# Performance work log

Hardware: AMD Instinct MI355X
Metric: run time of the kernel (lower is better)

## Reference

```python
import jax, jax.numpy as jnp
import numpy as np

N_HEAD, D_K, D_MODEL = 8, 64, 512  # factorized_k == d_k == d_v forced by view()/einsum consistency
B, LQ, LK = 4, 2048, 2048
TEMP = float(np.sqrt(D_K))
NEG = -1000000000.0


def setup_inputs() -> dict:
    key = jax.random.key(0)
    ks = jax.random.split(key, 8)
    q = jax.random.normal(ks[0], (B, LQ, D_MODEL), jnp.float32)
    k = jax.random.normal(ks[1], (B, LK, D_MODEL), jnp.float32)
    v = jax.random.normal(ks[2], (B, LK, D_MODEL), jnp.float32)
    mask = jax.random.randint(ks[3], (B, LQ, LK), 0, 2).astype(jnp.int32)
    # torch.rand-style positive uniform params, scaled to keep the 4-matmul chain O(1)
    W_A = jax.random.uniform(ks[4], (D_MODEL, D_K), jnp.float32, 0.0, 1.0 / D_K)
    W_A2 = jax.random.uniform(ks[5], (D_MODEL, D_K), jnp.float32, 0.0, 1.0 / D_K)
    W_A3 = jax.random.uniform(ks[6], (D_MODEL, D_K), jnp.float32, 0.0, 1.0 / D_K)
    fc_w = jax.random.normal(ks[7], (D_MODEL, N_HEAD * D_K), jnp.float32) / np.float32(np.sqrt(N_HEAD * D_K))
    ln_gamma = jnp.ones((D_MODEL,), jnp.float32)
    ln_beta = jnp.zeros((D_MODEL,), jnp.float32)
    return dict(q=q, k=k, v=v, mask=mask, W_A=W_A, W_A2=W_A2, W_A3=W_A3,
                fc_w=fc_w, ln_gamma=ln_gamma, ln_beta=ln_beta)


def reference(q, k, v, mask, W_A, W_A2, W_A3, fc_w, ln_gamma, ln_beta):
    b, lq, dm = q.shape
    lk = k.shape[1]
    residual = q
    # Since factorized_k == d_k, view(n_head,d_k,-1) and view(n_head,-1,d_k) coincide.
    W_a = W_A.reshape(N_HEAD, D_K, D_K)    # plays both 'bcd' (W_A) and 'bdi' (W_B)
    W_a2 = W_A2.reshape(N_HEAD, D_K, D_K)  # plays both 'bim' (W_At) and 'bmj' (W_Bt)
    W_av = W_A3.reshape(N_HEAD, D_K, D_K)  # plays both 'bna' (W_av) and 'bac' (W_bv)

    kt = jnp.swapaxes(k, 1, 2).reshape(b, N_HEAD, D_K, lk)  # [b,h,dk,lk]
    qh = q.reshape(b, lq, N_HEAD, D_K)                       # [b,lq,h,dk]
    vh = v.reshape(b, lk, N_HEAD, D_K)                       # [b,lk,h,dk]

    # Fold the tiny per-head weight chain first (same math as the 6-tensor einsum).
    Wq = jnp.einsum('hcd,hdi,him,hmj->hcj', W_a, W_a, W_a2, W_a2)  # [h,dk,dk]
    attn = jnp.einsum('kahc,hcj,khjn->khan', qh, Wq, kt) / TEMP     # [b,h,lq,lk]
    attn = jnp.where(mask[:, None, :, :] != 0, attn, NEG)
    attn = jax.nn.softmax(attn, axis=-1)  # dropout is identity in eval

    Wv = jnp.einsum('hna,hac->hnc', W_av, W_av)                    # [h,dk,dk]
    out = jnp.einsum('khjm,kmhn,hnc->khjc', attn, vh, Wv)          # [b,h,lq,dk]
    out = jnp.swapaxes(out, 1, 2).reshape(b, lq, N_HEAD * D_K)
    out = out @ fc_w.T  # Linear bias=False; dropout identity
    out = out + residual
    mu = jnp.mean(out, axis=-1, keepdims=True)
    var = jnp.mean((out - mu) ** 2, axis=-1, keepdims=True)
    out = (out - mu) / jnp.sqrt(var + 1e-6) * ln_gamma + ln_beta
    return (out, attn)
```

## Files before the change

### kernel.cpp

```cpp
#include <hip/hip_runtime.h>

#define B_ 4
#define H_ 8
#define L_ 2048
#define DM 512
#define DK 64

typedef __bf16 bf16x8 __attribute__((ext_vector_type(8)));
typedef float f32x4 __attribute__((ext_vector_type(4)));

__device__ __forceinline__ f32x4 mfma16(bf16x8 a, bf16x8 b, f32x4 c) {
  return __builtin_amdgcn_mfma_f32_16x16x32_bf16(a, b, c, 0, 0, 0);
}
__device__ __forceinline__ unsigned short f2bf(float f) {
  unsigned int u = __float_as_uint(f);
  u += 0x7fffu + ((u >> 16) & 1u);
  return (unsigned short)(u >> 16);
}
__device__ __forceinline__ void async16(const void* g, void* l) {
  __builtin_amdgcn_global_load_lds((const __attribute__((address_space(1))) unsigned int*)g,
                                   (__attribute__((address_space(3))) unsigned int*)l, 16, 0, 0);
}
__device__ __forceinline__ float rsum16(float v) {
  v += __shfl_xor(v, 1);
  v += __shfl_xor(v, 2);
  v += __shfl_xor(v, 4);
  v += __shfl_xor(v, 8);
  return v;
}

__device__ __forceinline__ void mm64(const float* X, const float* Y, float acc[4][4], int tr, int tc) {
#pragma unroll
  for (int rr = 0; rr < 4; ++rr)
#pragma unroll
    for (int cc = 0; cc < 4; ++cc) acc[rr][cc] = 0.f;
  for (int c = 0; c < 64; ++c) {
    float a0 = X[(tr + 0) * 65 + c], a1 = X[(tr + 1) * 65 + c];
    float a2 = X[(tr + 2) * 65 + c], a3 = X[(tr + 3) * 65 + c];
    float b0 = Y[c * 65 + tc + 0], b1 = Y[c * 65 + tc + 1];
    float b2 = Y[c * 65 + tc + 2], b3 = Y[c * 65 + tc + 3];
    acc[0][0] += a0 * b0; acc[0][1] += a0 * b1; acc[0][2] += a0 * b2; acc[0][3] += a0 * b3;
    acc[1][0] += a1 * b0; acc[1][1] += a1 * b1; acc[1][2] += a1 * b2; acc[1][3] += a1 * b3;
    acc[2][0] += a2 * b0; acc[2][1] += a2 * b1; acc[2][2] += a2 * b2; acc[2][3] += a2 * b3;
    acc[3][0] += a3 * b0; acc[3][1] += a3 * b1; acc[3][2] += a3 * b2; acc[3][3] += a3 * b3;
  }
}

__global__ __launch_bounds__(256) void k_weights(const float* __restrict__ WA, const float* __restrict__ WA2,
                                                 const float* __restrict__ WA3, float* __restrict__ Wq,
                                                 float* __restrict__ Wv) {
  __shared__ float sA[64 * 65], sB[64 * 65], sT[64 * 65];
  const int h = blockIdx.x, t = threadIdx.x;
  const int tr = (t >> 4) * 4, tc = (t & 15) * 4;
  for (int i = t; i < 4096; i += 256) {
    int r = i >> 6, c = i & 63;
    sA[r * 65 + c] = WA[h * 4096 + i];
    sB[r * 65 + c] = WA2[h * 4096 + i];
  }
  __syncthreads();
  float acc[4][4];
  mm64(sA, sA, acc, tr, tc);
#pragma unroll
  for (int rr = 0; rr < 4; ++rr)
#pragma unroll
    for (int cc = 0; cc < 4; ++cc) sT[(tr + rr) * 65 + tc + cc] = acc[rr][cc];
  __syncthreads();
  mm64(sT, sB, acc, tr, tc);
#pragma unroll
  for (int rr = 0; rr < 4; ++rr)
#pragma unroll
    for (int cc = 0; cc < 4; ++cc) sA[(tr + rr) * 65 + tc + cc] = acc[rr][cc];
  __syncthreads();
  mm64(sA, sB, acc, tr, tc);
#pragma unroll
  for (int rr = 0; rr < 4; ++rr)
#pragma unroll
    for (int cc = 0; cc < 4; ++cc) Wq[h * 4096 + (tr + rr) * 64 + tc + cc] = acc[rr][cc];
  for (int i = t; i < 4096; i += 256) {
    int r = i >> 6, c = i & 63;
    sT[r * 65 + c] = WA3[h * 4096 + i];
  }
  __syncthreads();
  mm64(sT, sT, acc, tr, tc);
#pragma unroll
  for (int rr = 0; rr < 4; ++rr)
#pragma unroll
    for (int cc = 0; cc < 4; ++cc) Wv[h * 4096 + (tr + rr) * 64 + tc + cc] = acc[rr][cc];
}

__global__ void k_conv(const float* __restrict__ s, unsigned short* __restrict__ d, int n4) {
  int i = blockIdx.x * blockDim.x + threadIdx.x;
  int stride = gridDim.x * blockDim.x;
  for (; i < n4; i += stride) {
    float4 f = ((const float4*)s)[i];
    ushort4 o;
    o.x = f2bf(f.x); o.y = f2bf(f.y); o.z = f2bf(f.z); o.w = f2bf(f.w);
    ((ushort4*)d)[i] = o;
  }
}

__global__ __launch_bounds__(256) void k_maskpack(const int* __restrict__ mask,
                                                  unsigned long long* __restrict__ mp) {
  const int row = blockIdx.x * 4 + (threadIdx.x >> 6);
  const int lane = threadIdx.x & 63;
  const int* src = mask + (size_t)row * L_;
#pragma unroll
  for (int c = 0; c < 32; ++c) {
    int mv = src[c * 64 + lane];
    unsigned long long bits = __ballot(mv != 0);
    if (lane == 0) mp[(size_t)row * 32 + c] = bits;
  }
}

__global__ __launch_bounds__(256) void k_qprime(const float* __restrict__ q, const float* __restrict__ Wq,
                                                unsigned short* __restrict__ Qp) {
  __shared__ float sW[64 * 65], sQ[64 * 65];
  const int bid = blockIdx.x;
  const int rt = bid & 31, h = (bid >> 5) & 7, b = bid >> 8;
  const int t = threadIdx.x;
  const int row0 = rt * 64;
  for (int i = t; i < 4096; i += 256) {
    int r = i >> 6, c = i & 63;
    sW[r * 65 + c] = Wq[h * 4096 + i];
    sQ[r * 65 + c] = q[(size_t)(b * L_ + row0 + r) * DM + h * DK + c];
  }
  __syncthreads();
  float acc[4][4];
  const int tr = (t >> 4) * 4, tc = (t & 15) * 4;
  mm64(sQ, sW, acc, tr, tc);
#pragma unroll
  for (int rr = 0; rr < 4; ++rr) {
    ushort4 o;
    o.x = f2bf(acc[rr][0] * 0.125f); o.y = f2bf(acc[rr][1] * 0.125f);
    o.z = f2bf(acc[rr][2] * 0.125f); o.w = f2bf(acc[rr][3] * 0.125f);
    *(ushort4*)&Qp[(size_t)(b * L_ + row0 + tr + rr) * DM + h * DK + tc] = o;
  }
}

__global__ __launch_bounds__(256) void k_vprime(const float* __restrict__ v, const float* __restrict__ Wv,
                                                unsigned short* __restrict__ VpT) {
  __shared__ float sW[64 * 65], sV[64 * 65];
  __shared__ __align__(16) unsigned short ldsT[64 * 72];
  const int bid = blockIdx.x;
  const int rt = bid & 31, h = (bid >> 5) & 7, b = bid >> 8;
  const int t = threadIdx.x;
  const int key0 = rt * 64;
  for (int i = t; i < 4096; i += 256) {
    int r = i >> 6, c = i & 63;
    sW[r * 65 + c] = Wv[h * 4096 + i];
    sV[r * 65 + c] = v[(size_t)(b * L_ + key0 + r) * DM + h * DK + c];
  }
  __syncthreads();
  float acc[4][4];
  const int tr = (t >> 4) * 4, tc = (t & 15) * 4;
  mm64(sV, sW, acc, tr, tc);
#pragma unroll
  for (int rr = 0; rr < 4; ++rr)
#pragma unroll
    for (int cc = 0; cc < 4; ++cc) ldsT[(tc + cc) * 72 + tr + rr] = f2bf(acc[rr][cc]);
  __syncthreads();
  const int dk = t >> 2, kc = t & 3;
  const uint4* srcp = (const uint4*)&ldsT[dk * 72 + kc * 16];
  uint4 v0 = srcp[0], v1 = srcp[1];
  size_t go = ((size_t)((b * H_ + h) * DK + dk)) * L_ + key0 + kc * 16;
  *(uint4*)&VpT[go] = v0;
  *(uint4*)&VpT[go + 8] = v1;
}

__global__ __launch_bounds__(256) void k_attn(const unsigned short* __restrict__ Qp,
                                              const unsigned short* __restrict__ Kb,
                                              const unsigned short* __restrict__ VpT,
                                              const unsigned long long* __restrict__ mp,
                                              float* __restrict__ attn,
                                              float* __restrict__ ov) {
  __shared__ __align__(16) unsigned short KT[2][4096];
  __shared__ __align__(16) unsigned short VT[2][4096];
  __shared__ __align__(16) unsigned short PB[4][16 * 76];
  const int bid0 = blockIdx.x;
  const int bid = (bid0 & 7) * 128 + (bid0 >> 3);
  const int qt = bid & 31;
  const int h = (bid >> 5) & 7;
  const int b = bid >> 8;
  const int tid = threadIdx.x;
  const int lane = tid & 63;
  const int w = tid >> 6;
  const int l15 = lane & 15, l4 = lane >> 4;
  const int row0 = qt * 64 + w * 16;

  const unsigned short* qb = Qp + ((size_t)(b * L_ + row0 + l15)) * DM + h * DK + l4 * 8;
  const bf16x8 aQ0 = *(const bf16x8*)qb;
  const bf16x8 aQ1 = *(const bf16x8*)(qb + 32);

  const size_t kb_base = (size_t)b * L_ * DM + h * DK;
  const size_t vt_base = (size_t)((b * H_ + h) * DK) * L_;
  const unsigned long long* mrow = mp + (size_t)(b * L_ + row0 + l4 * 4) * 32;

  const int p_lo = tid * 16;
  const int skey = p_lo >> 7;
  const int sboff = (p_lo & 127) ^ ((skey & 7) << 4);
  const int skey1 = (p_lo + 4096) >> 7;
  const int sboff1 = ((p_lo + 4096) & 127) ^ ((skey1 & 7) << 4);

#define STAGE_K(kt_, s_)                                                                   \
  {                                                                                        \
    async16(Kb + kb_base + (size_t)((kt_) * 64 + skey) * DM + (sboff >> 1),                \
            (char*)&KT[s_][0] + p_lo);                                                     \
    async16(Kb + kb_base + (size_t)((kt_) * 64 + skey1) * DM + (sboff1 >> 1),              \
            (char*)&KT[s_][0] + p_lo + 4096);                                              \
  }
#define STAGE_V(kt_, s_)                                                                   \
  {                                                                                        \
    async16(VpT + vt_base + (size_t)skey * L_ + (kt_) * 64 + (sboff >> 1),                 \
            (char*)&VT[s_][0] + p_lo);                                                     \
    async16(VpT + vt_base + (size_t)skey1 * L_ + (kt_) * 64 + (sboff1 >> 1),               \
            (char*)&VT[s_][0] + p_lo + 4096);                                              \
  }

  float lsum[4] = {0.f, 0.f, 0.f, 0.f};

  STAGE_K(0, 0);
  __syncthreads();
  for (int kt = 0; kt < 32; ++kt) {
    const int cur = kt & 1;
    if (kt < 31) STAGE_K(kt + 1, cur ^ 1);
    unsigned long long mw[4];
#pragma unroll
    for (int r = 0; r < 4; ++r) mw[r] = mrow[r * 32 + kt];
    const char* Kbase = (const char*)&KT[cur][0];
#pragma unroll
    for (int f = 0; f < 4; ++f) {
      int keyrow = f * 16 + l15;
      int sw = (keyrow & 7) << 4;
      bf16x8 b0 = *(const bf16x8*)(Kbase + keyrow * 128 + ((l4 * 16) ^ sw));
      bf16x8 b1 = *(const bf16x8*)(Kbase + keyrow * 128 + ((64 + l4 * 16) ^ sw));
      f32x4 acc = {0.f, 0.f, 0.f, 0.f};
      acc = mfma16(aQ0, b0, acc);
      acc = mfma16(aQ1, b1, acc);
#pragma unroll
      for (int r = 0; r < 4; ++r) {
        unsigned int hb = (unsigned int)(mw[r] >> (f * 16));
        lsum[r] += ((hb >> l15) & 1u) ? __expf(acc[r]) : 0.f;
      }
    }
    __syncthreads();
  }
  float invl[4];
#pragma unroll
  for (int r = 0; r < 4; ++r) invl[r] = 1.0f / rsum16(lsum[r]);

  f32x4 O[4];
#pragma unroll
  for (int d = 0; d < 4; ++d) { f32x4 z = {0.f, 0.f, 0.f, 0.f}; O[d] = z; }

  float* arow0 = attn + ((size_t)((b * H_ + h) * L_) + row0 + l4 * 4) * L_;

  STAGE_K(0, 0);
  STAGE_V(0, 0);
  __syncthreads();
  for (int kt = 0; kt < 32; ++kt) {
    const int cur = kt & 1;
    const int key0 = kt * 64;
    if (kt < 31) {
      STAGE_K(kt + 1, cur ^ 1);
      STAGE_V(kt + 1, cur ^ 1);
    }
    unsigned long long mw[4];
#pragma unroll
    for (int r = 0; r < 4; ++r) mw[r] = mrow[r * 32 + kt];
    const char* Kbase = (const char*)&KT[cur][0];
    const char* Vbase = (const char*)&VT[cur][0];
    float pv[4][4];
#pragma unroll
    for (int f = 0; f < 4; ++f) {
      int keyrow = f * 16 + l15;
      int sw = (keyrow & 7) << 4;
      bf16x8 b0 = *(const bf16x8*)(Kbase + keyrow * 128 + ((l4 * 16) ^ sw));
      bf16x8 b1 = *(const bf16x8*)(Kbase + keyrow * 128 + ((64 + l4 * 16) ^ sw));
      f32x4 acc = {0.f, 0.f, 0.f, 0.f};
      acc = mfma16(aQ0, b0, acc);
      acc = mfma16(aQ1, b1, acc);
#pragma unroll
      for (int r = 0; r < 4; ++r) {
        unsigned int hb = (unsigned int)(mw[r] >> (f * 16));
        pv[f][r] = ((hb >> l15) & 1u) ? __expf(acc[r]) * invl[r] : 0.f;
      }
    }
#pragma unroll
    for (int f = 0; f < 4; ++f)
#pragma unroll
      for (int r = 0; r < 4; ++r) {
        arow0[(size_t)r * L_ + key0 + f * 16 + l15] = pv[f][r];
        PB[w][(l4 * 4 + r) * 76 + f * 16 + l15] = f2bf(pv[f][r]);
      }
    bf16x8 aP0 = *(const bf16x8*)((const char*)&PB[w][0] + l15 * 152 + l4 * 16);
    bf16x8 aP1 = *(const bf16x8*)((const char*)&PB[w][0] + l15 * 152 + 64 + l4 * 16);
#pragma unroll
    for (int d = 0; d < 4; ++d) {
      int dkrow = d * 16 + l15;
      int sw = (dkrow & 7) << 4;
      bf16x8 v0 = *(const bf16x8*)(Vbase + dkrow * 128 + ((l4 * 16) ^ sw));
      bf16x8 v1 = *(const bf16x8*)(Vbase + dkrow * 128 + ((64 + l4 * 16) ^ sw));
      O[d] = mfma16(aP0, v0, O[d]);
      O[d] = mfma16(aP1, v1, O[d]);
    }
    __syncthreads();
  }
#pragma unroll
  for (int d = 0; d < 4; ++d)
#pragma unroll
    for (int r = 0; r < 4; ++r)
      ov[(size_t)(b * L_ + row0 + l4 * 4 + r) * DM + h * DK + d * 16 + l15] = O[d][r];
#undef STAGE_K
#undef STAGE_V
}

__global__ __launch_bounds__(256) void k_proj(const float* __restrict__ qres,
                                              const unsigned short* __restrict__ fcb,
                                              const float* __restrict__ gamma,
                                              const float* __restrict__ beta,
                                              float* __restrict__ io) {
  __shared__ float red1[16][4], red2[16][4];
  const int blk = blockIdx.x;
  const int tid = threadIdx.x, lane = tid & 63, w = tid >> 6;
  const int l15 = lane & 15, l4 = lane >> 4;
  const int row0 = blk * 16;
  const float* arow = io + (size_t)(row0 + l15) * DM + l4 * 8;
  const unsigned short* bb = fcb + (size_t)(w * 128 + l15) * DM + l4 * 8;
  f32x4 C[8];
#pragma unroll
  for (int i = 0; i < 8; ++i) { f32x4 z = {0.f, 0.f, 0.f, 0.f}; C[i] = z; }
  for (int kc = 0; kc < 16; ++kc) {
    float4 a0 = *(const float4*)(arow + kc * 32);
    float4 a1 = *(const float4*)(arow + kc * 32 + 4);
    union { unsigned short u[8]; bf16x8 v; } t;
    t.u[0] = f2bf(a0.x); t.u[1] = f2bf(a0.y); t.u[2] = f2bf(a0.z); t.u[3] = f2bf(a0.w);
    t.u[4] = f2bf(a1.x); t.u[5] = f2bf(a1.y); t.u[6] = f2bf(a1.z); t.u[7] = f2bf(a1.w);
#pragma unroll
    for (int cf = 0; cf < 8; ++cf) {
      bf16x8 bv = *(const bf16x8*)(bb + (size_t)(cf * 16) * DM + kc * 32);
      C[cf] = mfma16(t.v, bv, C[cf]);
    }
  }
  float s1[4] = {0.f, 0.f, 0.f, 0.f}, s2[4] = {0.f, 0.f, 0.f, 0.f};
  const int colb = w * 128;
#pragma unroll
  for (int cf = 0; cf < 8; ++cf)
#pragma unroll
    for (int r = 0; r < 4; ++r) {
      float val = C[cf][r] + qres[(size_t)(row0 + l4 * 4 + r) * DM + colb + cf * 16 + l15];
      C[cf][r] = val;
      s1[r] += val;
      s2[r] += val * val;
    }
#pragma unroll
  for (int r = 0; r < 4; ++r) { s1[r] = rsum16(s1[r]); s2[r] = rsum16(s2[r]); }
  if (l15 == 0) {
#pragma unroll
    for (int r = 0; r < 4; ++r) { red1[l4 * 4 + r][w] = s1[r]; red2[l4 * 4 + r][w] = s2[r]; }
  }
  __syncthreads();
  float mu[4], rs[4];
#pragma unroll
  for (int r = 0; r < 4; ++r) {
    int row = l4 * 4 + r;
    float t1 = red1[row][0] + red1[row][1] + red1[row][2] + red1[row][3];
    float t2 = red2[row][0] + red2[row][1] + red2[row][2] + red2[row][3];
    float m_ = t1 * (1.0f / 512.0f);
    float var = t2 * (1.0f / 512.0f) - m_ * m_;
    mu[r] = m_;
    rs[r] = rsqrtf(var + 1e-6f);
  }
#pragma unroll
  for (int cf = 0; cf < 8; ++cf) {
    float g = gamma[colb + cf * 16 + l15];
    float be = beta[colb + cf * 16 + l15];
#pragma unroll
    for (int r = 0; r < 4; ++r)
      io[(size_t)(row0 + l4 * 4 + r) * DM + colb + cf * 16 + l15] =
          (C[cf][r] - mu[r]) * rs[r] * g + be;
  }
}

extern "C" void kernel_launch(void* const* d_in, const int* in_sizes, int n_in,
                              void* d_out, int out_size, void* d_ws, size_t ws_size,
                              hipStream_t stream) {
  (void)in_sizes; (void)n_in; (void)out_size; (void)ws_size;
  const float* q   = (const float*)d_in[0];
  const float* k   = (const float*)d_in[1];
  const float* v   = (const float*)d_in[2];
  const int* mask  = (const int*)d_in[3];
  const float* WA  = (const float*)d_in[4];
  const float* WA2 = (const float*)d_in[5];
  const float* WA3 = (const float*)d_in[6];
  const float* fcw = (const float*)d_in[7];
  const float* gam = (const float*)d_in[8];
  const float* bet = (const float*)d_in[9];
  float* out = (float*)d_out;
  float* attn = out + (size_t)B_ * L_ * DM;

  char* ws = (char*)d_ws;
  float* Wq = (float*)ws;
  float* Wv = (float*)(ws + 131072);
  unsigned short* Qp  = (unsigned short*)(ws + 262144);
  unsigned short* Kb  = (unsigned short*)(ws + 262144 + 8388608);
  unsigned short* VpT = (unsigned short*)(ws + 262144 + 2 * 8388608);
  unsigned short* FCb = (unsigned short*)(ws + 262144 + 3 * 8388608);
  unsigned long long* mp = (unsigned long long*)(ws + 262144 + 3 * 8388608 + 524288);

  k_weights<<<8, 256, 0, stream>>>(WA, WA2, WA3, Wq, Wv);
  k_conv<<<1024, 256, 0, stream>>>(k, Kb, (B_ * L_ * DM) / 4);
  k_conv<<<256, 256, 0, stream>>>(fcw, FCb, (DM * DM) / 4);
  k_maskpack<<<2048, 256, 0, stream>>>(mask, mp);
  k_qprime<<<1024, 256, 0, stream>>>(q, Wq, Qp);
  k_vprime<<<1024, 256, 0, stream>>>(v, Wv, VpT);
  k_attn<<<1024, 256, 0, stream>>>(Qp, Kb, VpT, mp, attn, out);
  k_proj<<<512, 256, 0, stream>>>(q, FCb, gam, bet, out);
}
```

Before: 372.8 us.

## Hand-pipeline attention loops with explicit vmcnt waits, mask prefetch, and exp2

Restructures both attention passes so mask words are prefetched two tiles ahead, async K/V staging is synchronized with explicit s_waitcnt vmcnt counts and raw s_barrier instead of __syncthreads, and scheduling barriers pin the instruction order. Folds log2(e) into the Q scaling so exp2f replaces __expf. Attention-probability stores become nontemporal and the PV MFMA block is run at raised wave priority. The aim is to overlap global loads with compute and cut barrier and store costs. The vmcnt counts must match the number of outstanding loads and stores, so any miscount risks a race.

Measured after the change: 330.2 us. -11.4%, faster.

```diff
diff --git a/kernel.cpp b/kernel.cpp
--- a/kernel.cpp
+++ b/kernel.cpp
@@ -119,6 +119,7 @@
   const int rt = bid & 31, h = (bid >> 5) & 7, b = bid >> 8;
   const int t = threadIdx.x;
   const int row0 = rt * 64;
+  const float QS = 0.125f * 1.44269504088896f;
   for (int i = t; i < 4096; i += 256) {
     int r = i >> 6, c = i & 63;
     sW[r * 65 + c] = Wq[h * 4096 + i];
@@ -131,8 +132,8 @@
 #pragma unroll
   for (int rr = 0; rr < 4; ++rr) {
     ushort4 o;
-    o.x = f2bf(acc[rr][0] * 0.125f); o.y = f2bf(acc[rr][1] * 0.125f);
-    o.z = f2bf(acc[rr][2] * 0.125f); o.w = f2bf(acc[rr][3] * 0.125f);
+    o.x = f2bf(acc[rr][0] * QS); o.y = f2bf(acc[rr][1] * QS);
+    o.z = f2bf(acc[rr][2] * QS); o.w = f2bf(acc[rr][3] * QS);
     *(ushort4*)&Qp[(size_t)(b * L_ + row0 + tr + rr) * DM + h * DK + tc] = o;
   }
 }
@@ -216,34 +217,51 @@
             (char*)&VT[s_][0] + p_lo + 4096);                                              \
   }
 
+  unsigned long long mwA[4], mwB[4];
   float lsum[4] = {0.f, 0.f, 0.f, 0.f};
 
+#pragma unroll
+  for (int r = 0; r < 4; ++r) { mwA[r] = mrow[r * 32 + 0]; mwB[r] = mrow[r * 32 + 1]; }
   STAGE_K(0, 0);
-  __syncthreads();
-  for (int kt = 0; kt < 32; ++kt) {
-    const int cur = kt & 1;
-    if (kt < 31) STAGE_K(kt + 1, cur ^ 1);
-    unsigned long long mw[4];
-#pragma unroll
-    for (int r = 0; r < 4; ++r) mw[r] = mrow[r * 32 + kt];
-    const char* Kbase = (const char*)&KT[cur][0];
-#pragma unroll
-    for (int f = 0; f < 4; ++f) {
-      int keyrow = f * 16 + l15;
-      int sw = (keyrow & 7) << 4;
-      bf16x8 b0 = *(const bf16x8*)(Kbase + keyrow * 128 + ((l4 * 16) ^ sw));
-      bf16x8 b1 = *(const bf16x8*)(Kbase + keyrow * 128 + ((64 + l4 * 16) ^ sw));
-      f32x4 acc = {0.f, 0.f, 0.f, 0.f};
-      acc = mfma16(aQ0, b0, acc);
-      acc = mfma16(aQ1, b1, acc);
-#pragma unroll
-      for (int r = 0; r < 4; ++r) {
-        unsigned int hb = (unsigned int)(mw[r] >> (f * 16));
-        lsum[r] += ((hb >> l15) & 1u) ? __expf(acc[r]) : 0.f;
-      }
-    }
-    __syncthreads();
-  }
+  asm volatile("s_waitcnt vmcnt(0)" ::: "memory");
+  __builtin_amdgcn_s_barrier();
+
+#define P1_BODY(KT_, VMN_, DO_STAGE_, DO_LOADM_)                                           \
+  {                                                                                        \
+    const int kt = (KT_);                                                                  \
+    const int cur = kt & 1;                                                                \
+    __builtin_amdgcn_sched_barrier(0);                                                     \
+    unsigned long long mwN[4] = {0ull, 0ull, 0ull, 0ull};                                  \
+    if (DO_LOADM_) {                                                                       \
+      _Pragma("unroll") for (int r = 0; r < 4; ++r) mwN[r] = mrow[r * 32 + kt + 2];        \
+    }                                                                                      \
+    if (DO_STAGE_) STAGE_K(kt + 1, cur ^ 1);                                               \
+    asm volatile("s_waitcnt vmcnt(" #VMN_ ")" ::: "memory");                               \
+    __builtin_amdgcn_sched_barrier(0);                                                     \
+    __builtin_amdgcn_s_barrier();                                                          \
+    const char* Kbase = (const char*)&KT[cur][0];                                          \
+    _Pragma("unroll") for (int f = 0; f < 4; ++f) {                                        \
+      int keyrow = f * 16 + l15;                                                           \
+      int sw = (keyrow & 7) << 4;                                                          \
+      bf16x8 b0 = *(const bf16x8*)(Kbase + keyrow * 128 + ((l4 * 16) ^ sw));               \
+      bf16x8 b1 = *(const bf16x8*)(Kbase + keyrow * 128 + ((64 + l4 * 16) ^ sw));          \
+      f32x4 acc = {0.f, 0.f, 0.f, 0.f};                                                    \
+      acc = mfma16(aQ0, b0, acc);                                                          \
+      acc = mfma16(aQ1, b1, acc);                                                          \
+      _Pragma("unroll") for (int r = 0; r < 4; ++r) {                                      \
+        unsigned int hb = (unsigned int)(mwA[r] >> (f * 16));                              \
+        lsum[r] += ((hb >> l15) & 1u) ? exp2f(acc[r]) : 0.f;                               \
+      }                                                                                    \
+    }                                                                                      \
+    __builtin_amdgcn_s_barrier();                                                          \
+    _Pragma("unroll") for (int r = 0; r < 4; ++r) { mwA[r] = mwB[r]; mwB[r] = mwN[r]; }    \
+  }
+
+  for (int t = 0; t < 30; ++t) P1_BODY(t, 6, true, true);
+  P1_BODY(30, 2, true, false);
+  P1_BODY(31, 0, false, false);
+#undef P1_BODY
+
   float invl[4];
 #pragma unroll
   for (int r = 0; r < 4; ++r) invl[r] = 1.0f / rsum16(lsum[r]);
@@ -254,57 +272,71 @@
 
   float* arow0 = attn + ((size_t)((b * H_ + h) * L_) + row0 + l4 * 4) * L_;
 
+#pragma unroll
+  for (int r = 0; r < 4; ++r) { mwA[r] = mrow[r * 32 + 0]; mwB[r] = mrow[r * 32 + 1]; }
   STAGE_K(0, 0);
   STAGE_V(0, 0);
-  __syncthreads();
-  for (int kt = 0; kt < 32; ++kt) {
-    const int cur = kt & 1;
-    const int key0 = kt * 64;
-    if (kt < 31) {
-      STAGE_K(kt + 1, cur ^ 1);
-      STAGE_V(kt + 1, cur ^ 1);
-    }
-    unsigned long long mw[4];
-#pragma unroll
-    for (int r = 0; r < 4; ++r) mw[r] = mrow[r * 32 + kt];
-    const char* Kbase = (const char*)&KT[cur][0];
-    const char* Vbase = (const char*)&VT[cur][0];
-    float pv[4][4];
-#pragma unroll
-    for (int f = 0; f < 4; ++f) {
-      int keyrow = f * 16 + l15;
-      int sw = (keyrow & 7) << 4;
-      bf16x8 b0 = *(const bf16x8*)(Kbase + keyrow * 128 + ((l4 * 16) ^ sw));
-      bf16x8 b1 = *(const bf16x8*)(Kbase + keyrow * 128 + ((64 + l4 * 16) ^ sw));
-      f32x4 acc = {0.f, 0.f, 0.f, 0.f};
-      acc = mfma16(aQ0, b0, acc);
-      acc = mfma16(aQ1, b1, acc);
-#pragma unroll
-      for (int r = 0; r < 4; ++r) {
-        unsigned int hb = (unsigned int)(mw[r] >> (f * 16));
-        pv[f][r] = ((hb >> l15) & 1u) ? __expf(acc[r]) * invl[r] : 0.f;
-      }
-    }
-#pragma unroll
-    for (int f = 0; f < 4; ++f)
-#pragma unroll
-      for (int r = 0; r < 4; ++r) {
-        arow0[(size_t)r * L_ + key0 + f * 16 + l15] = pv[f][r];
-        PB[w][(l4 * 4 + r) * 76 + f * 16 + l15] = f2bf(pv[f][r]);
-      }
-    bf16x8 aP0 = *(const bf16x8*)((const char*)&PB[w][0] + l15 * 152 + l4 * 16);
-    bf16x8 aP1 = *(const bf16x8*)((const char*)&PB[w][0] + l15 * 152 + 64 + l4 * 16);
-#pragma unroll
-    for (int d = 0; d < 4; ++d) {
-      int dkrow = d * 16 + l15;
-      int sw = (dkrow & 7) << 4;
-      bf16x8 v0 = *(const bf16x8*)(Vbase + dkrow * 128 + ((l4 * 16) ^ sw));
-      bf16x8 v1 = *(const bf16x8*)(Vbase + dkrow * 128 + ((64 + l4 * 16) ^ sw));
-      O[d] = mfma16(aP0, v0, O[d]);
-      O[d] = mfma16(aP1, v1, O[d]);
-    }
-    __syncthreads();
-  }
+  asm volatile("s_waitcnt vmcnt(0)" ::: "memory");
+  __builtin_amdgcn_s_barrier();
+
+#define P2_BODY(KT_, VMN_, DO_STAGE_, DO_LOADM_)                                           \
+  {                                                                                        \
+    const int kt = (KT_);                                                                  \
+    const int cur = kt & 1;                                                                \
+    const int key0 = kt * 64;                                                              \
+    __builtin_amdgcn_sched_barrier(0);                                                     \
+    unsigned long long mwN[4] = {0ull, 0ull, 0ull, 0ull};                                  \
+    if (DO_LOADM_) {                                                                       \
+      _Pragma("unroll") for (int r = 0; r < 4; ++r) mwN[r] = mrow[r * 32 + kt + 2];        \
+    }                                                                                      \
+    if (DO_STAGE_) { STAGE_K(kt + 1, cur ^ 1); STAGE_V(kt + 1, cur ^ 1); }                 \
+    asm volatile("s_waitcnt vmcnt(" #VMN_ ")" ::: "memory");                               \
+    __builtin_amdgcn_sched_barrier(0);                                                     \
+    __builtin_amdgcn_s_barrier();                                                          \
+    const char* Kbase = (const char*)&KT[cur][0];                                          \
+    const char* Vbase = (const char*)&VT[cur][0];                                          \
+    float pvv[4][4];                                                                       \
+    _Pragma("unroll") for (int f = 0; f < 4; ++f) {                                        \
+      int keyrow = f * 16 + l15;                                                           \
+      int sw = (keyrow & 7) << 4;                                                          \
+      bf16x8 b0 = *(const bf16x8*)(Kbase + keyrow * 128 + ((l4 * 16) ^ sw));               \
+      bf16x8 b1 = *(const bf16x8*)(Kbase + keyrow * 128 + ((64 + l4 * 16) ^ sw));          \
+      f32x4 acc = {0.f, 0.f, 0.f, 0.f};                                                    \
+      acc = mfma16(aQ0, b0, acc);                                                          \
+      acc = mfma16(aQ1, b1, acc);                                                          \
+      _Pragma("unroll") for (int r = 0; r < 4; ++r) {                                      \
+        unsigned int hb = (unsigned int)(mwA[r] >> (f * 16));                              \
+        pvv[f][r] = ((hb >> l15) & 1u) ? exp2f(acc[r]) * invl[r] : 0.f;                    \
+      }                                                                                    \
+    }                                                                                      \
+    _Pragma("unroll") for (int f = 0; f < 4; ++f)                                          \
+      _Pragma("unroll") for (int r = 0; r < 4; ++r)                                        \
+        __builtin_nontemporal_store(pvv[f][r],                                             \
+            arow0 + (size_t)r * L_ + key0 + f * 16 + l15);                                 \
+    _Pragma("unroll") for (int f = 0; f < 4; ++f)                                          \
+      _Pragma("unroll") for (int r = 0; r < 4; ++r)                                        \
+        PB[w][(l4 * 4 + r) * 76 + f * 16 + l15] = f2bf(pvv[f][r]);                         \
+    bf16x8 aP0 = *(const bf16x8*)((const char*)&PB[w][0] + l15 * 152 + l4 * 16);           \
+    bf16x8 aP1 = *(const bf16x8*)((const char*)&PB[w][0] + l15 * 152 + 64 + l4 * 16);      \
+    __builtin_amdgcn_s_setprio(1);                                                         \
+    _Pragma("unroll") for (int d = 0; d < 4; ++d) {                                        \
+      int dkrow = d * 16 + l15;                                                            \
+      int sw = (dkrow & 7) << 4;                                                           \
+      bf16x8 v0 = *(const bf16x8*)(Vbase + dkrow * 128 + ((l4 * 16) ^ sw));                \
+      bf16x8 v1 = *(const bf16x8*)(Vbase + dkrow * 128 + ((64 + l4 * 16) ^ sw));           \
+      O[d] = mfma16(aP0, v0, O[d]);                                                        \
+      O[d] = mfma16(aP1, v1, O[d]);                                                        \
+    }                                                                                      \
+    __builtin_amdgcn_s_setprio(0);                                                         \
+    __builtin_amdgcn_s_barrier();                                                          \
+    _Pragma("unroll") for (int r = 0; r < 4; ++r) { mwA[r] = mwB[r]; mwB[r] = mwN[r]; }    \
+  }
+
+  for (int t = 0; t < 30; ++t) P2_BODY(t, 24, true, true);
+  P2_BODY(30, 20, true, false);
+  P2_BODY(31, 16, false, false);
+#undef P2_BODY
+
 #pragma unroll
   for (int d = 0; d < 4; ++d)
 #pragma unroll
```
